# Performance work log

Hardware: AMD Instinct MI355X
Metric: run time of the kernel (lower is better)

Reference implementation:

```python
import jax, jax.numpy as jnp
import numpy as np

N, D, E = 100000, 64, 1250000  # nodes, feature dim, total signed edges
H = D // 2                     # per-polarity hidden dim


def _mean_agg(x, src, dst, n):
    """Mean-aggregate messages x[src] at dst over n segments (gather->scatter)."""
    s = jax.ops.segment_sum(x[src], dst, num_segments=n)
    cnt = jax.ops.segment_sum(jnp.ones((src.shape[0], 1), x.dtype), dst, num_segments=n)
    return s / jnp.maximum(cnt, 1.0)


def _lin_w(k, fi, fo):
    b = 1.0 / np.sqrt(fi)
    return jax.random.uniform(k, (fi, fo), jnp.float32, -b, b)


def setup_inputs() -> dict:
    key = jax.random.key(0)
    ks = list(jax.random.split(key, 24))
    init_emb = jax.random.normal(ks[0], (N, D), dtype=jnp.float32)
    src = jax.random.randint(ks[1], (E,), 0, N)
    dst = jax.random.randint(ks[2], (E,), 0, N)
    sign = jnp.where(jax.random.uniform(ks[3], (E,)) < 0.5, 1, -1)
    edge_index_s = jnp.stack([src, dst, sign], axis=1)
    return dict(
        init_emb=init_emb,
        edge_index_s=edge_index_s,
        # conv1 (first_aggr=True): lin([mean_agg, x]) per polarity -> H
        Wp1=_lin_w(ks[4], 2 * D, H), bp1=jnp.zeros((H,), jnp.float32),
        Wn1=_lin_w(ks[5], 2 * D, H), bn1=jnp.zeros((H,), jnp.float32),
        # rest conv: lin([agg_pos, agg_neg, x_half]) per polarity -> H
        Wp2=_lin_w(ks[6], 3 * H, H), bp2=jnp.zeros((H,), jnp.float32),
        Wn2=_lin_w(ks[7], 3 * H, H), bn2=jnp.zeros((H,), jnp.float32),
        # final linear D->D
        Ww=_lin_w(ks[8], D, D), bw=jnp.zeros((D,), jnp.float32),
        # MLP readout: Linear+BN+ReLU, Linear+BN+ReLU, Linear->1 (inference mode)
        Wm1=_lin_w(ks[9], D, D), bm1=jnp.zeros((D,), jnp.float32),
        g1=jnp.ones((D,), jnp.float32), be1=jnp.zeros((D,), jnp.float32),
        rm1=jnp.zeros((D,), jnp.float32), rv1=jnp.ones((D,), jnp.float32),
        Wm2=_lin_w(ks[10], D, D), bm2=jnp.zeros((D,), jnp.float32),
        g2=jnp.ones((D,), jnp.float32), be2=jnp.zeros((D,), jnp.float32),
        rm2=jnp.zeros((D,), jnp.float32), rv2=jnp.ones((D,), jnp.float32),
        Wm3=_lin_w(ks[11], D, 1), bm3=jnp.zeros((1,), jnp.float32),
    )


def reference(init_emb, edge_index_s, Wp1, bp1, Wn1, bn1, Wp2, bp2, Wn2, bn2,
              Ww, bw, Wm1, bm1, g1, be1, rm1, rv1, Wm2, bm2, g2, be2, rm2, rv2,
              Wm3, bm3):
    # split signed edge list into pos / neg edge indices (eager boolean mask,
    # mirrors edge_index_s[edge_index_s[:,2]>0][:, :2].t())
    sign = edge_index_s[:, 2]
    pos = edge_index_s[sign > 0]
    neg = edge_index_s[sign < 0]
    ps, pd = pos[:, 0], pos[:, 1]
    ns, nd = neg[:, 0], neg[:, 1]

    x = init_emb
    # --- first signed conv (first_aggr=True) ---
    ap = _mean_agg(x, ps, pd, N)
    an = _mean_agg(x, ns, nd, N)
    hp = jnp.concatenate([ap, x], -1) @ Wp1 + bp1
    hn = jnp.concatenate([an, x], -1) @ Wn1 + bn1
    z = jnp.tanh(jnp.concatenate([hp, hn], -1))  # [N, D]

    # --- rest signed conv (balance-theory cross-polarity aggregation) ---
    xp, xn = z[:, :H], z[:, H:]
    hp = jnp.concatenate([_mean_agg(xp, ps, pd, N), _mean_agg(xn, ns, nd, N), xp], -1) @ Wp2 + bp2
    hn = jnp.concatenate([_mean_agg(xn, ps, pd, N), _mean_agg(xp, ns, nd, N), xn], -1) @ Wn2 + bn2
    z = jnp.tanh(jnp.concatenate([hp, hn], -1))  # [N, D]

    # --- final linear + tanh ---
    z = jnp.tanh(z @ Ww + bw)

    # --- MLP readout (inference: BN uses running stats, dropout disabled) ---
    def bn(h, g, b, rm, rv):
        return (h - rm) * jax.lax.rsqrt(rv + 1e-5) * g + b

    h = jax.nn.relu(bn(z @ Wm1 + bm1, g1, be1, rm1, rv1))
    h = jax.nn.relu(bn(h @ Wm2 + bm2, g2, be2, rm2, rv2))
    prob = jax.nn.sigmoid(h @ Wm3 + bm3)  # [N, 1]
    return z, prob
```

## Files before the change

kernel.cpp:

```cpp
#include <hip/hip_runtime.h>
#include <hip/hip_bf16.h>

#define CAP 32

typedef __attribute__((ext_vector_type(8))) short bf16x8;
typedef __attribute__((ext_vector_type(4))) float f32x4;

#define MFMA(a, b, c) __builtin_amdgcn_mfma_f32_16x16x32_bf16(a, b, c, 0, 0, 0)

__device__ __forceinline__ unsigned short bf16rn(float f) {
    unsigned u = __builtin_bit_cast(unsigned, f);
    u += 0x7fffu + ((u >> 16) & 1u);
    return (unsigned short)(u >> 16);
}

__device__ __forceinline__ bf16x8 packbf8(const float* p) {
    bf16x8 r;
    #pragma unroll
    for (int j = 0; j < 8; ++j) r[j] = (short)bf16rn(p[j]);
    return r;
}

__device__ __forceinline__ bf16x8 wfrag(const float* __restrict__ W, int NN,
                                        int kt, int ct, int q, int c) {
    const float* base = W + (kt * 32 + q * 8) * NN + ct * 16 + c;
    float t[8];
    #pragma unroll
    for (int j = 0; j < 8; ++j) t[j] = base[j * NN];
    return packbf8(t);
}

__device__ __forceinline__ bf16x8 afrag_bf16(const __hip_bfloat16* row, int cw, int q) {
    return *(const bf16x8*)((const short*)row + cw + q * 8);
}

__global__ __launch_bounds__(256) void pg_cast(
    const float* __restrict__ x, __hip_bfloat16* __restrict__ xb, int n)
{
    int i = (blockIdx.x * 256 + threadIdx.x) * 4;
    if (i < n) {
        float4 v = *(const float4*)(x + i);
        ushort4 o;
        o.x = bf16rn(v.x); o.y = bf16rn(v.y);
        o.z = bf16rn(v.z); o.w = bf16rn(v.w);
        *(ushort4*)((unsigned short*)xb + i) = o;
    }
}

__global__ __launch_bounds__(256) void pg_build(
    const int* __restrict__ ei,
    int* __restrict__ plist, int* __restrict__ nlist,
    int* __restrict__ pcur, int* __restrict__ ncur, int E)
{
    int e = blockIdx.x * 256 + threadIdx.x;
    if (e >= E) return;
    int s  = ei[3 * e + 0];
    int d  = ei[3 * e + 1];
    int sg = ei[3 * e + 2];
    int* cur  = (sg > 0) ? pcur : ncur;
    int* list = (sg > 0) ? plist : nlist;
    int slot = atomicAdd(cur + d, 1);
    if (slot < CAP) list[(size_t)d * CAP + slot] = s;
}

__global__ __launch_bounds__(256, 6) void pg_gather(
    const __hip_bfloat16* __restrict__ src,
    const int* __restrict__ plist, const int* __restrict__ nlist,
    const int* __restrict__ pcur, const int* __restrict__ ncur,
    __hip_bfloat16* __restrict__ agg, int N)
{
    int tid = threadIdx.x;
    int w = tid >> 6, lane = tid & 63;

    #pragma unroll 1
    for (int g = 0; g < 4; ++g) {
        int i0 = blockIdx.x * 64 + w * 16 + g * 4;
        int pd[4], nd[4], pde[4], nde[4], pl[4], nl[4];
        #pragma unroll
        for (int n = 0; n < 4; ++n) {
            int i = min(i0 + n, N - 1);
            pd[n] = __builtin_amdgcn_readfirstlane(pcur[i]);
            nd[n] = __builtin_amdgcn_readfirstlane(ncur[i]);
            pde[n] = min(pd[n], CAP);
            nde[n] = min(nd[n], CAP);
            const int* plrow = plist + (size_t)i * CAP;
            const int* nlrow = nlist + (size_t)i * CAP;
            pl[n] = plrow[lane & 31];
            nl[n] = nlrow[lane & 31];
        }
        int maxd = 0;
        #pragma unroll
        for (int n = 0; n < 4; ++n) maxd = max(maxd, max(pde[n], nde[n]));

        float ps[4] = {0.f, 0.f, 0.f, 0.f}, ns[4] = {0.f, 0.f, 0.f, 0.f};
        #pragma unroll 1
        for (int e = 0; e < maxd; e += 4) {
            float pv[4][4], nv[4][4];
            #pragma unroll
            for (int n = 0; n < 4; ++n) {
                #pragma unroll
                for (int k = 0; k < 4; ++k) {
                    int idx = e + k;
                    int psl = (idx < pde[n]) ? idx : 0;
                    int nsl = (idx < nde[n]) ? idx : 0;
                    unsigned sp = (unsigned)__builtin_amdgcn_readlane(pl[n], psl);
                    unsigned sn = (unsigned)__builtin_amdgcn_readlane(nl[n], nsl);
                    sp = sp < (unsigned)N ? sp : 0u;
                    sn = sn < (unsigned)N ? sn : 0u;
                    const __hip_bfloat16* prow = src + ((size_t)sp << 6);
                    const __hip_bfloat16* nrow = src + ((size_t)sn << 6);
                    pv[n][k] = __bfloat162float(prow[lane]);
                    nv[n][k] = __bfloat162float(nrow[lane]);
                }
            }
            #pragma unroll
            for (int n = 0; n < 4; ++n) {
                #pragma unroll
                for (int k = 0; k < 4; ++k) {
                    int idx = e + k;
                    float wp  = (idx < pde[n]) ? 1.f : 0.f;
                    float wn_ = (idx < nde[n]) ? 1.f : 0.f;
                    ps[n] = fmaf(wp,  pv[n][k], ps[n]);
                    ns[n] = fmaf(wn_, nv[n][k], ns[n]);
                }
            }
        }
        #pragma unroll
        for (int n = 0; n < 4; ++n) {
            int i = i0 + n;
            if (i < N) {
                __hip_bfloat16* arow = agg + ((size_t)i << 7);
                arow[lane]      = __float2bfloat16(ps[n] / fmaxf((float)pd[n], 1.f));
                arow[64 + lane] = __float2bfloat16(ns[n] / fmaxf((float)nd[n], 1.f));
            }
        }
    }
}

__global__ __launch_bounds__(256, 3) void pg_gemm1(
    const __hip_bfloat16* __restrict__ xb, const __hip_bfloat16* __restrict__ agg,
    const float* __restrict__ Wp, const float* __restrict__ bp,
    const float* __restrict__ Wn, const float* __restrict__ bn,
    __hip_bfloat16* __restrict__ z1b, int N, int nwv)
{
    int tid = threadIdx.x;
    int w = tid >> 6, lane = tid & 63;
    int q = lane >> 4, c = lane & 15;

    bf16x8 B[2][4][2];
    #pragma unroll
    for (int kt = 0; kt < 4; ++kt)
        #pragma unroll
        for (int ct = 0; ct < 2; ++ct) {
            B[0][kt][ct] = wfrag(Wp, 32, kt, ct, q, c);
            B[1][kt][ct] = wfrag(Wn, 32, kt, ct, q, c);
        }
    float bias[2][2];
    #pragma unroll
    for (int ct = 0; ct < 2; ++ct) {
        bias[0][ct] = bp[ct * 16 + c];
        bias[1][ct] = bn[ct * 16 + c];
    }

    int ntiles = (N + 15) >> 4;
    #pragma unroll 1
    for (int t = blockIdx.x * 4 + w; t < ntiles; t += nwv) {
        int i = min(t * 16 + c, N - 1);
        const __hip_bfloat16* arow = agg + ((size_t)i << 7);
        const __hip_bfloat16* xrow = xb + ((size_t)i << 6);
        bf16x8 aA0 = afrag_bf16(arow, 0, q);
        bf16x8 aA1 = afrag_bf16(arow, 32, q);
        bf16x8 aA2 = afrag_bf16(arow, 64, q);
        bf16x8 aA3 = afrag_bf16(arow, 96, q);
        bf16x8 aX0 = afrag_bf16(xrow, 0, q);
        bf16x8 aX1 = afrag_bf16(xrow, 32, q);
        f32x4 acc[2][2];
        #pragma unroll
        for (int ct = 0; ct < 2; ++ct) {
            f32x4 a = {0.f, 0.f, 0.f, 0.f};
            a = MFMA(aA0, B[0][0][ct], a);
            a = MFMA(aA1, B[0][1][ct], a);
            a = MFMA(aX0, B[0][2][ct], a);
            a = MFMA(aX1, B[0][3][ct], a);
            acc[0][ct] = a;
            f32x4 b = {0.f, 0.f, 0.f, 0.f};
            b = MFMA(aA2, B[1][0][ct], b);
            b = MFMA(aA3, B[1][1][ct], b);
            b = MFMA(aX0, B[1][2][ct], b);
            b = MFMA(aX1, B[1][3][ct], b);
            acc[1][ct] = b;
        }
        #pragma unroll
        for (int h = 0; h < 2; ++h)
            #pragma unroll
            for (int ct = 0; ct < 2; ++ct)
                #pragma unroll
                for (int r = 0; r < 4; ++r) {
                    int row = t * 16 + q * 4 + r;
                    if (row < N)
                        z1b[(size_t)row * 64 + h * 32 + ct * 16 + c] =
                            __float2bfloat16(tanhf(acc[h][ct][r] + bias[h][ct]));
                }
    }
}

__global__ __launch_bounds__(256, 3) void pg_gemm2(
    const __hip_bfloat16* __restrict__ z1b, __hip_bfloat16* agg,
    const float* __restrict__ Wp2, const float* __restrict__ bp2,
    const float* __restrict__ Wn2, const float* __restrict__ bn2,
    int N, int nwv)
{
    int tid = threadIdx.x;
    int w = tid >> 6, lane = tid & 63;
    int q = lane >> 4, c = lane & 15;

    bf16x8 B[2][3][2];
    #pragma unroll
    for (int kt = 0; kt < 3; ++kt)
        #pragma unroll
        for (int ct = 0; ct < 2; ++ct) {
            B[0][kt][ct] = wfrag(Wp2, 32, kt, ct, q, c);
            B[1][kt][ct] = wfrag(Wn2, 32, kt, ct, q, c);
        }
    float bias[2][2];
    #pragma unroll
    for (int ct = 0; ct < 2; ++ct) {
        bias[0][ct] = bp2[ct * 16 + c];
        bias[1][ct] = bn2[ct * 16 + c];
    }

    int ntiles = (N + 15) >> 4;
    #pragma unroll 1
    for (int t = blockIdx.x * 4 + w; t < ntiles; t += nwv) {
        int i = min(t * 16 + c, N - 1);
        const __hip_bfloat16* arow = agg + ((size_t)i << 7);
        const __hip_bfloat16* zrow = z1b + ((size_t)i << 6);
        bf16x8 ap0 = afrag_bf16(arow, 0, q);
        bf16x8 ap1 = afrag_bf16(arow, 96, q);
        bf16x8 an0 = afrag_bf16(arow, 32, q);
        bf16x8 an1 = afrag_bf16(arow, 64, q);
        bf16x8 az0 = afrag_bf16(zrow, 0, q);
        bf16x8 az1 = afrag_bf16(zrow, 32, q);
        f32x4 acc[2][2];
        #pragma unroll
        for (int ct = 0; ct < 2; ++ct) {
            f32x4 a = {0.f, 0.f, 0.f, 0.f};
            a = MFMA(ap0, B[0][0][ct], a);
            a = MFMA(ap1, B[0][1][ct], a);
            a = MFMA(az0, B[0][2][ct], a);
            acc[0][ct] = a;
            f32x4 b = {0.f, 0.f, 0.f, 0.f};
            b = MFMA(an0, B[1][0][ct], b);
            b = MFMA(an1, B[1][1][ct], b);
            b = MFMA(az1, B[1][2][ct], b);
            acc[1][ct] = b;
        }
        #pragma unroll
        for (int h = 0; h < 2; ++h)
            #pragma unroll
            for (int ct = 0; ct < 2; ++ct)
                #pragma unroll
                for (int r = 0; r < 4; ++r) {
                    int row = t * 16 + q * 4 + r;
                    if (row < N)
                        agg[(size_t)row * 128 + h * 32 + ct * 16 + c] =
                            __float2bfloat16(tanhf(acc[h][ct][r] + bias[h][ct]));
                }
    }
}

__global__ __launch_bounds__(256, 2) void pg_mlp(
    float* out, const __hip_bfloat16* __restrict__ z2b,
    const float* __restrict__ Ww,  const float* __restrict__ bw,
    const float* __restrict__ Wm1, const float* __restrict__ bm1,
    const float* __restrict__ g1,  const float* __restrict__ be1,
    const float* __restrict__ rm1, const float* __restrict__ rv1,
    const float* __restrict__ Wm2, const float* __restrict__ bm2,
    const float* __restrict__ g2,  const float* __restrict__ be2,
    const float* __restrict__ rm2, const float* __restrict__ rv2,
    const float* __restrict__ Wm3, const float* __restrict__ bm3,
    int N, int nwv)
{
    __shared__ float xpos[4][16][68];
    int tid = threadIdx.x;
    int w = tid >> 6, lane = tid & 63;
    int q = lane >> 4, c = lane & 15;
    float (*lx)[68] = xpos[w];

    bf16x8 Bw[2][4], B1[2][4], B2[2][4];
    #pragma unroll
    for (int kt = 0; kt < 2; ++kt)
        #pragma unroll
        for (int ct = 0; ct < 4; ++ct) {
            Bw[kt][ct] = wfrag(Ww,  64, kt, ct, q, c);
            B1[kt][ct] = wfrag(Wm1, 64, kt, ct, q, c);
            B2[kt][ct] = wfrag(Wm2, 64, kt, ct, q, c);
        }
    float bwv[4], s1[4], o1[4], s2[4], o2[4], w3[4];
    #pragma unroll
    for (int ct = 0; ct < 4; ++ct) {
        int cc = ct * 16 + c;
        bwv[ct] = bw[cc];
        float a = g1[cc] * rsqrtf(rv1[cc] + 1e-5f);
        s1[ct] = a; o1[ct] = (bm1[cc] - rm1[cc]) * a + be1[cc];
        float b = g2[cc] * rsqrtf(rv2[cc] + 1e-5f);
        s2[ct] = b; o2[ct] = (bm2[cc] - rm2[cc]) * b + be2[cc];
        w3[ct] = Wm3[cc];
    }
    float b3 = bm3[0];

    int ntiles = (N + 15) >> 4;
    #pragma unroll 1
    for (int t = blockIdx.x * 4 + w; t < ntiles; t += nwv) {
        int i = min(t * 16 + c, N - 1);
        const __hip_bfloat16* zrow = z2b + ((size_t)i << 7);
        bf16x8 a0 = afrag_bf16(zrow, 0, q);
        bf16x8 a1 = afrag_bf16(zrow, 32, q);
        f32x4 acc[4];

        #pragma unroll
        for (int ct = 0; ct < 4; ++ct) {
            f32x4 a = {0.f, 0.f, 0.f, 0.f};
            a = MFMA(a0, Bw[0][ct], a);
            a = MFMA(a1, Bw[1][ct], a);
            acc[ct] = a;
        }
        #pragma unroll
        for (int ct = 0; ct < 4; ++ct)
            #pragma unroll
            for (int r = 0; r < 4; ++r) {
                int row = t * 16 + q * 4 + r;
                float v = tanhf(acc[ct][r] + bwv[ct]);
                if (row < N) out[(size_t)row * 64 + ct * 16 + c] = v;
                lx[q * 4 + r][ct * 16 + c] = v;
            }
        {
            const float* pr = &lx[c][0];
            float tb[8];
            *(float4*)tb       = *(const float4*)(pr + q * 8);
            *(float4*)(tb + 4) = *(const float4*)(pr + q * 8 + 4);
            a0 = packbf8(tb);
            *(float4*)tb       = *(const float4*)(pr + 32 + q * 8);
            *(float4*)(tb + 4) = *(const float4*)(pr + 32 + q * 8 + 4);
            a1 = packbf8(tb);
        }

        #pragma unroll
        for (int ct = 0; ct < 4; ++ct) {
            f32x4 a = {0.f, 0.f, 0.f, 0.f};
            a = MFMA(a0, B1[0][ct], a);
            a = MFMA(a1, B1[1][ct], a);
            acc[ct] = a;
        }
        #pragma unroll
        for (int ct = 0; ct < 4; ++ct)
            #pragma unroll
            for (int r = 0; r < 4; ++r)
                lx[q * 4 + r][ct * 16 + c] = fmaxf(acc[ct][r] * s1[ct] + o1[ct], 0.f);
        {
            const float* pr = &lx[c][0];
            float tb[8];
            *(float4*)tb       = *(const float4*)(pr + q * 8);
            *(float4*)(tb + 4) = *(const float4*)(pr + q * 8 + 4);
            a0 = packbf8(tb);
            *(float4*)tb       = *(const float4*)(pr + 32 + q * 8);
            *(float4*)(tb + 4) = *(const float4*)(pr + 32 + q * 8 + 4);
            a1 = packbf8(tb);
        }

        #pragma unroll
        for (int ct = 0; ct < 4; ++ct) {
            f32x4 a = {0.f, 0.f, 0.f, 0.f};
            a = MFMA(a0, B2[0][ct], a);
            a = MFMA(a1, B2[1][ct], a);
            acc[ct] = a;
        }
        float tr[4];
        #pragma unroll
        for (int r = 0; r < 4; ++r) {
            float hs = 0.f;
            #pragma unroll
            for (int ct = 0; ct < 4; ++ct) {
                float h2 = fmaxf(acc[ct][r] * s2[ct] + o2[ct], 0.f);
                hs = fmaf(h2, w3[ct], hs);
            }
            tr[r] = hs;
        }
        #pragma unroll
        for (int m = 1; m < 16; m <<= 1)
            #pragma unroll
            for (int r = 0; r < 4; ++r) tr[r] += __shfl_xor(tr[r], m, 16);
        if (c == 0) {
            #pragma unroll
            for (int r = 0; r < 4; ++r) {
                int row = t * 16 + q * 4 + r;
                if (row < N)
                    out[(size_t)N * 64 + row] = 1.f / (1.f + expf(-(tr[r] + b3)));
            }
        }
    }
}

extern "C" void kernel_launch(void* const* d_in, const int* in_sizes, int n_in,
                              void* d_out, int out_size, void* d_ws, size_t ws_size,
                              hipStream_t stream) {
    const float* x   = (const float*)d_in[0];
    const int*   ei  = (const int*)  d_in[1];
    const float* Wp1 = (const float*)d_in[2];
    const float* bp1 = (const float*)d_in[3];
    const float* Wn1 = (const float*)d_in[4];
    const float* bn1 = (const float*)d_in[5];
    const float* Wp2 = (const float*)d_in[6];
    const float* bp2 = (const float*)d_in[7];
    const float* Wn2 = (const float*)d_in[8];
    const float* bn2 = (const float*)d_in[9];
    const float* Ww  = (const float*)d_in[10];
    const float* bw  = (const float*)d_in[11];
    const float* Wm1 = (const float*)d_in[12];
    const float* bm1 = (const float*)d_in[13];
    const float* g1  = (const float*)d_in[14];
    const float* be1 = (const float*)d_in[15];
    const float* rm1 = (const float*)d_in[16];
    const float* rv1 = (const float*)d_in[17];
    const float* Wm2 = (const float*)d_in[18];
    const float* bm2 = (const float*)d_in[19];
    const float* g2  = (const float*)d_in[20];
    const float* be2 = (const float*)d_in[21];
    const float* rm2 = (const float*)d_in[22];
    const float* rv2 = (const float*)d_in[23];
    const float* Wm3 = (const float*)d_in[24];
    const float* bm3 = (const float*)d_in[25];
    float* out = (float*)d_out;

    int N = in_sizes[0] / 64;
    int E = in_sizes[1] / 3;

    int* plist = (int*)d_ws;
    int* nlist = plist + (size_t)N * CAP;
    int* pcur  = nlist + (size_t)N * CAP;
    int* ncur  = pcur + N;
    __hip_bfloat16* agg = (__hip_bfloat16*)(ncur + N);

    __hip_bfloat16* z1b = (__hip_bfloat16*)out;
    __hip_bfloat16* xb  = (__hip_bfloat16*)((char*)d_out + (size_t)N * 128);

    pg_cast<<<(N * 64 / 4 + 255) / 256, 256, 0, stream>>>(x, xb, N * 64);

    hipMemsetAsync(pcur, 0, 2 * (size_t)N * sizeof(int), stream);
    pg_build<<<(E + 255) / 256, 256, 0, stream>>>(ei, plist, nlist, pcur, ncur, E);

    int nb = (N + 63) / 64;
    const int gb = 512, nwv = gb * 4;
    pg_gather<<<nb, 256, 0, stream>>>(xb, plist, nlist, pcur, ncur, agg, N);
    pg_gemm1<<<gb, 256, 0, stream>>>(xb, agg, Wp1, bp1, Wn1, bn1, z1b, N, nwv);
    pg_gather<<<nb, 256, 0, stream>>>(z1b, plist, nlist, pcur, ncur, agg, N);
    pg_gemm2<<<gb, 256, 0, stream>>>(z1b, agg, Wp2, bp2, Wn2, bn2, N, nwv);
    pg_mlp<<<gb, 256, 0, stream>>>(out, agg, Ww, bw,
                                   Wm1, bm1, g1, be1, rm1, rv1,
                                   Wm2, bm2, g2, be2, rm2, rv2,
                                   Wm3, bm3, N, nwv);
}
```

Measured before the change: 257.4 us.

## Fuse cast into edge build, batch atomics, and vectorize gather across edge groups

The bf16 cast of the input embeddings is merged into the edge-bucketing kernel, so one launch covers both and each build thread handles four edges with batched atomics. The gather kernel now splits each wave into four 16-lane groups. Each group loads one neighbor row with 8-byte vector loads (four bf16 values per lane), so a wave processes four edges at once instead of issuing one 2-byte load per lane per edge. Partial sums are combined with cross-group shuffles and stored packed. This trades extra shuffle reductions and more registers for far fewer scalar memory instructions in the gather loop.

```diff
diff --git a/kernel.cpp b/kernel.cpp
--- a/kernel.cpp
+++ b/kernel.cpp
@@ -14,6 +14,16 @@
     return (unsigned short)(u >> 16);
 }
 
+__device__ __forceinline__ float bf16lo(unsigned u) {
+    return __builtin_bit_cast(float, u << 16);
+}
+__device__ __forceinline__ float bf16hi(unsigned u) {
+    return __builtin_bit_cast(float, u & 0xffff0000u);
+}
+__device__ __forceinline__ unsigned pack2(float a, float b) {
+    return (unsigned)bf16rn(a) | ((unsigned)bf16rn(b) << 16);
+}
+
 __device__ __forceinline__ bf16x8 packbf8(const float* p) {
     bf16x8 r;
     #pragma unroll
@@ -34,33 +44,47 @@
     return *(const bf16x8*)((const short*)row + cw + q * 8);
 }
 
-__global__ __launch_bounds__(256) void pg_cast(
-    const float* __restrict__ x, __hip_bfloat16* __restrict__ xb, int n)
-{
-    int i = (blockIdx.x * 256 + threadIdx.x) * 4;
-    if (i < n) {
-        float4 v = *(const float4*)(x + i);
-        ushort4 o;
-        o.x = bf16rn(v.x); o.y = bf16rn(v.y);
-        o.z = bf16rn(v.z); o.w = bf16rn(v.w);
-        *(ushort4*)((unsigned short*)xb + i) = o;
-    }
-}
-
-__global__ __launch_bounds__(256) void pg_build(
+__global__ __launch_bounds__(256) void pg_build_cast(
     const int* __restrict__ ei,
     int* __restrict__ plist, int* __restrict__ nlist,
-    int* __restrict__ pcur, int* __restrict__ ncur, int E)
+    int* __restrict__ pcur, int* __restrict__ ncur, int E, int buildBlocks,
+    const float* __restrict__ x, __hip_bfloat16* __restrict__ xb, int nx)
 {
-    int e = blockIdx.x * 256 + threadIdx.x;
-    if (e >= E) return;
-    int s  = ei[3 * e + 0];
-    int d  = ei[3 * e + 1];
-    int sg = ei[3 * e + 2];
-    int* cur  = (sg > 0) ? pcur : ncur;
-    int* list = (sg > 0) ? plist : nlist;
-    int slot = atomicAdd(cur + d, 1);
-    if (slot < CAP) list[(size_t)d * CAP + slot] = s;
+    int b = blockIdx.x;
+    if (b >= buildBlocks) {
+        int i = ((b - buildBlocks) * 256 + threadIdx.x) * 4;
+        if (i < nx) {
+            float4 v = *(const float4*)(x + i);
+            ushort4 o;
+            o.x = bf16rn(v.x); o.y = bf16rn(v.y);
+            o.z = bf16rn(v.z); o.w = bf16rn(v.w);
+            *(ushort4*)((unsigned short*)xb + i) = o;
+        }
+        return;
+    }
+    int e0 = (b * 256 + threadIdx.x) * 4;
+    int s[4], d[4], sg[4];
+    bool ok[4];
+    #pragma unroll
+    for (int k = 0; k < 4; ++k) {
+        int e = e0 + k;
+        ok[k] = (e < E);
+        int ee = ok[k] ? e : 0;
+        s[k]  = ei[3 * ee + 0];
+        d[k]  = ei[3 * ee + 1];
+        sg[k] = ei[3 * ee + 2];
+    }
+    int slot[4];
+    int* dstl[4];
+    #pragma unroll
+    for (int k = 0; k < 4; ++k) {
+        int* cur = (sg[k] > 0) ? pcur : ncur;
+        dstl[k]  = ((sg[k] > 0) ? plist : nlist) + (size_t)d[k] * CAP;
+        slot[k]  = ok[k] ? atomicAdd(cur + d[k], 1) : CAP;
+    }
+    #pragma unroll
+    for (int k = 0; k < 4; ++k)
+        if (slot[k] < CAP) dstl[k][slot[k]] = s[k];
 }
 
 __global__ __launch_bounds__(256, 6) void pg_gather(
@@ -71,6 +95,8 @@
 {
     int tid = threadIdx.x;
     int w = tid >> 6, lane = tid & 63;
+    int grp = lane >> 4;
+    int q   = lane & 15;
 
     #pragma unroll 1
     for (int g = 0; g < 4; ++g) {
@@ -83,55 +109,74 @@
             nd[n] = __builtin_amdgcn_readfirstlane(ncur[i]);
             pde[n] = min(pd[n], CAP);
             nde[n] = min(nd[n], CAP);
-            const int* plrow = plist + (size_t)i * CAP;
-            const int* nlrow = nlist + (size_t)i * CAP;
-            pl[n] = plrow[lane & 31];
-            nl[n] = nlrow[lane & 31];
+            pl[n] = plist[(size_t)i * CAP + (lane & 31)];
+            nl[n] = nlist[(size_t)i * CAP + (lane & 31)];
         }
         int maxd = 0;
         #pragma unroll
         for (int n = 0; n < 4; ++n) maxd = max(maxd, max(pde[n], nde[n]));
 
-        float ps[4] = {0.f, 0.f, 0.f, 0.f}, ns[4] = {0.f, 0.f, 0.f, 0.f};
+        float ps[4][4], ns[4][4];
+        #pragma unroll
+        for (int n = 0; n < 4; ++n)
+            #pragma unroll
+            for (int r = 0; r < 4; ++r) { ps[n][r] = 0.f; ns[n][r] = 0.f; }
+
         #pragma unroll 1
         for (int e = 0; e < maxd; e += 4) {
-            float pv[4][4], nv[4][4];
             #pragma unroll
             for (int n = 0; n < 4; ++n) {
-                #pragma unroll
-                for (int k = 0; k < 4; ++k) {
-                    int idx = e + k;
-                    int psl = (idx < pde[n]) ? idx : 0;
-                    int nsl = (idx < nde[n]) ? idx : 0;
-                    unsigned sp = (unsigned)__builtin_amdgcn_readlane(pl[n], psl);
-                    unsigned sn = (unsigned)__builtin_amdgcn_readlane(nl[n], nsl);
-                    sp = sp < (unsigned)N ? sp : 0u;
-                    sn = sn < (unsigned)N ? sn : 0u;
-                    const __hip_bfloat16* prow = src + ((size_t)sp << 6);
-                    const __hip_bfloat16* nrow = src + ((size_t)sn << 6);
-                    pv[n][k] = __bfloat162float(prow[lane]);
-                    nv[n][k] = __bfloat162float(nrow[lane]);
-                }
+                int p0 = __builtin_amdgcn_readlane(pl[n], (e + 0) < pde[n] ? e + 0 : 0);
+                int p1 = __builtin_amdgcn_readlane(pl[n], (e + 1) < pde[n] ? e + 1 : 0);
+                int p2 = __builtin_amdgcn_readlane(pl[n], (e + 2) < pde[n] ? e + 2 : 0);
+                int p3 = __builtin_amdgcn_readlane(pl[n], (e + 3) < pde[n] ? e + 3 : 0);
+                int m0 = __builtin_amdgcn_readlane(nl[n], (e + 0) < nde[n] ? e + 0 : 0);
+                int m1 = __builtin_amdgcn_readlane(nl[n], (e + 1) < nde[n] ? e + 1 : 0);
+                int m2 = __builtin_amdgcn_readlane(nl[n], (e + 2) < nde[n] ? e + 2 : 0);
+                int m3 = __builtin_amdgcn_readlane(nl[n], (e + 3) < nde[n] ? e + 3 : 0);
+                unsigned sp = (unsigned)(grp == 0 ? p0 : grp == 1 ? p1 : grp == 2 ? p2 : p3);
+                unsigned sn = (unsigned)(grp == 0 ? m0 : grp == 1 ? m1 : grp == 2 ? m2 : m3);
+                sp = sp < (unsigned)N ? sp : 0u;
+                sn = sn < (unsigned)N ? sn : 0u;
+                uint2 pv = *((const uint2*)(src + ((size_t)sp << 6)) + q);
+                uint2 nv = *((const uint2*)(src + ((size_t)sn << 6)) + q);
+                float wp  = (e + grp < pde[n]) ? 1.f : 0.f;
+                float wn_ = (e + grp < nde[n]) ? 1.f : 0.f;
+                ps[n][0] = fmaf(wp, bf16lo(pv.x), ps[n][0]);
+                ps[n][1] = fmaf(wp, bf16hi(pv.x), ps[n][1]);
+                ps[n][2] = fmaf(wp, bf16lo(pv.y), ps[n][2]);
+                ps[n][3] = fmaf(wp, bf16hi(pv.y), ps[n][3]);
+                ns[n][0] = fmaf(wn_, bf16lo(nv.x), ns[n][0]);
+                ns[n][1] = fmaf(wn_, bf16hi(nv.x), ns[n][1]);
+                ns[n][2] = fmaf(wn_, bf16lo(nv.y), ns[n][2]);
+                ns[n][3] = fmaf(wn_, bf16hi(nv.y), ns[n][3]);
             }
-            #pragma unroll
-            for (int n = 0; n < 4; ++n) {
-                #pragma unroll
-                for (int k = 0; k < 4; ++k) {
-                    int idx = e + k;
-                    float wp  = (idx < pde[n]) ? 1.f : 0.f;
-                    float wn_ = (idx < nde[n]) ? 1.f : 0.f;
-                    ps[n] = fmaf(wp,  pv[n][k], ps[n]);
-                    ns[n] = fmaf(wn_, nv[n][k], ns[n]);
-                }
+        }
+        #pragma unroll
+        for (int n = 0; n < 4; ++n) {
+            #pragma unroll
+            for (int r = 0; r < 4; ++r) {
+                ps[n][r] += __shfl_xor(ps[n][r], 16);
+                ps[n][r] += __shfl_xor(ps[n][r], 32);
+                ns[n][r] += __shfl_xor(ns[n][r], 16);
+                ns[n][r] += __shfl_xor(ns[n][r], 32);
             }
-        }
-        #pragma unroll
-        for (int n = 0; n < 4; ++n) {
             int i = i0 + n;
             if (i < N) {
-                __hip_bfloat16* arow = agg + ((size_t)i << 7);
-                arow[lane]      = __float2bfloat16(ps[n] / fmaxf((float)pd[n], 1.f));
-                arow[64 + lane] = __float2bfloat16(ns[n] / fmaxf((float)nd[n], 1.f));
+                float invp = 1.f / fmaxf((float)pd[n], 1.f);
+                float invn = 1.f / fmaxf((float)nd[n], 1.f);
+                uint2* arow = (uint2*)(agg + ((size_t)i << 7));
+                if (grp == 0) {
+                    uint2 ow;
+                    ow.x = pack2(ps[n][0] * invp, ps[n][1] * invp);
+                    ow.y = pack2(ps[n][2] * invp, ps[n][3] * invp);
+                    arow[q] = ow;
+                } else if (grp == 1) {
+                    uint2 ow;
+                    ow.x = pack2(ns[n][0] * invn, ns[n][1] * invn);
+                    ow.y = pack2(ns[n][2] * invn, ns[n][3] * invn);
+                    arow[16 + q] = ow;
+                }
             }
         }
     }
@@ -444,10 +489,12 @@
     __hip_bfloat16* z1b = (__hip_bfloat16*)out;
     __hip_bfloat16* xb  = (__hip_bfloat16*)((char*)d_out + (size_t)N * 128);
 
-    pg_cast<<<(N * 64 / 4 + 255) / 256, 256, 0, stream>>>(x, xb, N * 64);
-
     hipMemsetAsync(pcur, 0, 2 * (size_t)N * sizeof(int), stream);
-    pg_build<<<(E + 255) / 256, 256, 0, stream>>>(ei, plist, nlist, pcur, ncur, E);
+
+    int buildBlocks = (E + 1023) / 1024;
+    int castBlocks  = (N * 64 / 4 + 255) / 256;
+    pg_build_cast<<<buildBlocks + castBlocks, 256, 0, stream>>>(
+        ei, plist, nlist, pcur, ncur, E, buildBlocks, x, xb, N * 64);
 
     int nb = (N + 63) / 64;
     const int gb = 512, nwv = gb * 4;
```

New measurement: 258.2 us. About the same (+0.3%).
